# Kernel optimization log

Measured on AMD Instinct MI355X. Metric: run time of the kernel, lower is better.

## Reference

```python
import jax, jax.numpy as jnp
import numpy as np

N_QUBITS = 4
DIM = 16
N_QLAYERS = 2

def _cnot_perm(c, t):
    idx = np.arange(DIM)
    cbit = (idx >> (N_QUBITS - 1 - c)) & 1
    return np.where(cbit == 1, idx ^ (1 << (N_QUBITS - 1 - t)), idx)

# ring entanglement: CNOT(0,1), CNOT(1,2), CNOT(2,3), CNOT(3,0)
RING_PERMS = [jnp.asarray(_cnot_perm(i, (i + 1) % N_QUBITS)) for i in range(N_QUBITS)]
_idx = np.arange(DIM)
ZSIGNS = jnp.asarray(np.stack([1.0 - 2.0 * ((_idx >> (N_QUBITS - 1 - q)) & 1) for q in range(N_QUBITS)], axis=1).astype(np.float32))  # (16, 4)

def _rx(t):
    c = jnp.cos(t / 2).astype(jnp.complex64)
    s = jnp.sin(t / 2).astype(jnp.complex64)
    return jnp.stack([jnp.stack([c, -1j * s]), jnp.stack([-1j * s, c])])

def _ry(t):
    c = jnp.cos(t / 2).astype(jnp.complex64)
    s = jnp.sin(t / 2).astype(jnp.complex64)
    return jnp.stack([jnp.stack([c, -s]), jnp.stack([s, c])])

def _rz(t):
    e = jnp.exp(-0.5j * t.astype(jnp.complex64))
    z = jnp.zeros((), jnp.complex64)
    return jnp.stack([jnp.stack([e, z]), jnp.stack([z, jnp.conj(e)])])

def _apply_1q(state, g, q):
    # wire 0 is the most significant bit (PennyLane convention)
    s = state.reshape(2 ** q, 2, 2 ** (N_QUBITS - 1 - q))
    return jnp.einsum('ij,ajc->aic', g, s).reshape(DIM)

def _circuit(angles, qw):
    # angles: (4,), qw: (n_qlayers, 4, 3); returns PauliZ expvals (4,)
    state = jnp.zeros(DIM, jnp.complex64).at[0].set(1.0)
    for q in range(N_QUBITS):
        state = _apply_1q(state, _ry(angles[q]), q)
    for l in range(N_QLAYERS):
        for q in range(N_QUBITS):
            state = _apply_1q(state, _rx(qw[l, q, 0]), q)
            state = _apply_1q(state, _ry(qw[l, q, 1]), q)
            state = _apply_1q(state, _rz(qw[l, q, 2]), q)
        for p in RING_PERMS:
            state = state[p]
    probs = jnp.abs(state) ** 2
    return probs @ ZSIGNS

def _conv(x, w, b, stride, pad):
    y = jax.lax.conv_general_dilated(x, w, (stride, stride), [(pad, pad), (pad, pad)], dimension_numbers=('NCHW', 'OIHW', 'NCHW'))
    return y + b[None, :, None, None]

def _bn(x, g, b, m, v):
    scale = (g / jnp.sqrt(v + 1e-5))[None, :, None, None]
    return (x - m[None, :, None, None]) * scale + b[None, :, None, None]

def _forward(x, c1w, c1b, bn1g, bn1b, bn1m, bn1v, c2w, c2b, bn2g, bn2b, bn2m, bn2v, c3w, c3b, bn3g, bn3b, bn3m, bn3v, pre_w, pre_b, qw, pw1, pb1, pw2, pb2):
    B = x.shape[0]
    h = jax.nn.relu(_bn(_conv(x, c1w, c1b, 4, 3), bn1g, bn1b, bn1m, bn1v))   # (B,32,56,56)
    h = jax.nn.relu(_bn(_conv(h, c2w, c2b, 2, 1), bn2g, bn2b, bn2m, bn2v))   # (B,64,28,28)
    h = jax.nn.relu(_bn(_conv(h, c3w, c3b, 2, 1), bn3g, bn3b, bn3m, bn3v))   # (B,128,14,14)
    h = h.reshape(B, 128, 2, 7, 2, 7).mean(axis=(3, 5))                       # AdaptiveAvgPool2d((2,2))
    f = h.reshape(B, 128 * 4)
    ang = jnp.tanh(f @ pre_w.T + pre_b) * jnp.pi                              # (B,4)
    qout = jax.vmap(lambda a: _circuit(a, qw))(ang)                            # (B,4) batched statevector sim
    h1 = jax.nn.relu(qout @ pw1.T + pb1)                                       # dropout inactive (eval)
    return h1 @ pw2.T + pb2

def setup_inputs() -> dict:
    key = jax.random.key(0)
    ks = jax.random.split(key, 16)
    d = {
        'x': jax.random.normal(ks[0], (128, 3, 224, 224), jnp.float32),
        'c1w': jax.random.normal(ks[1], (32, 3, 7, 7), jnp.float32) * 0.05,
        'c1b': jax.random.normal(ks[2], (32,), jnp.float32) * 0.05,
        'bn1g': jnp.ones((32,), jnp.float32), 'bn1b': jnp.zeros((32,), jnp.float32),
        'bn1m': jnp.zeros((32,), jnp.float32), 'bn1v': jnp.ones((32,), jnp.float32),
        'c2w': jax.random.normal(ks[3], (64, 32, 3, 3), jnp.float32) * 0.05,
        'c2b': jax.random.normal(ks[4], (64,), jnp.float32) * 0.05,
        'bn2g': jnp.ones((64,), jnp.float32), 'bn2b': jnp.zeros((64,), jnp.float32),
        'bn2m': jnp.zeros((64,), jnp.float32), 'bn2v': jnp.ones((64,), jnp.float32),
        'c3w': jax.random.normal(ks[5], (128, 64, 3, 3), jnp.float32) * 0.05,
        'c3b': jax.random.normal(ks[6], (128,), jnp.float32) * 0.05,
        'bn3g': jnp.ones((128,), jnp.float32), 'bn3b': jnp.zeros((128,), jnp.float32),
        'bn3m': jnp.zeros((128,), jnp.float32), 'bn3v': jnp.ones((128,), jnp.float32),
        'pre_w': jax.random.normal(ks[7], (4, 512), jnp.float32) * 0.04,
        'pre_b': jax.random.normal(ks[8], (4,), jnp.float32) * 0.04,
        'qw': jax.random.normal(ks[9], (2, 4, 3), jnp.float32) * 0.1,
        'pw1': jax.random.normal(ks[10], (64, 4), jnp.float32) * 0.5,
        'pb1': jax.random.normal(ks[11], (64,), jnp.float32) * 0.5,
        'pw2': jax.random.normal(ks[12], (5, 64), jnp.float32) * 0.12,
        'pb2': jax.random.normal(ks[13], (5,), jnp.float32) * 0.12,
    }
    return d

def reference(x, c1w, c1b, bn1g, bn1b, bn1m, bn1v, c2w, c2b, bn2g, bn2b, bn2m, bn2v, c3w, c3b, bn3g, bn3b, bn3m, bn3v, pre_w, pre_b, qw, pw1, pb1, pw2, pb2):
    return _forward(x, c1w, c1b, bn1g, bn1b, bn1m, bn1v, c2w, c2b, bn2g, bn2b, bn2m, bn2v, c3w, c3b, bn3g, bn3b, bn3m, bn3v, pre_w, pre_b, qw, pw1, pb1, pw2, pb2)
```

## Files before the change

### kernel.cpp

```cpp
#include <hip/hip_runtime.h>
#include <math.h>

#define DEV __device__ __forceinline__

typedef __attribute__((ext_vector_type(8))) __bf16 bf16x8;
typedef __attribute__((ext_vector_type(4))) float f32x4;

__global__ void prep_weights(
    const float* __restrict__ c1w, const float* __restrict__ c1b,
    const float* __restrict__ g1, const float* __restrict__ b1,
    const float* __restrict__ m1, const float* __restrict__ v1,
    const float* __restrict__ c2w, const float* __restrict__ c2b,
    const float* __restrict__ g2, const float* __restrict__ b2,
    const float* __restrict__ m2, const float* __restrict__ v2,
    const float* __restrict__ c3w, const float* __restrict__ c3b,
    const float* __restrict__ g3, const float* __restrict__ b3,
    const float* __restrict__ m3, const float* __restrict__ v3,
    __bf16* __restrict__ wb1, __bf16* __restrict__ wb2, __bf16* __restrict__ wb3,
    float* __restrict__ sc1, float* __restrict__ sh1,
    float* __restrict__ sc2, float* __restrict__ sh2,
    float* __restrict__ sc3, float* __restrict__ sh3)
{
    int gid = blockIdx.x * 256 + threadIdx.x;
    int gs = gridDim.x * 256;
    for (int e = gid; e < 32 * 192; e += gs) {
        int oc = e / 192, k = e % 192, rr = k >> 3, kw = k & 7;
        wb1[e] = (rr < 21 && kw >= 1) ? (__bf16)c1w[oc * 147 + rr * 7 + kw - 1]
                                      : (__bf16)0.f;
    }
    for (int e = gid; e < 64 * 384; e += gs) {
        int oc = e / 384, k = e % 384, rr = k >> 2, kw = k & 3;
        wb2[e] = (kw >= 1) ? (__bf16)c2w[oc * 288 + rr * 3 + kw - 1] : (__bf16)0.f;
    }
    for (int e = gid; e < 128 * 768; e += gs) {
        int oc = e / 768, k = e % 768, rr = k >> 2, kw = k & 3;
        wb3[e] = (kw >= 1) ? (__bf16)c3w[oc * 576 + rr * 3 + kw - 1] : (__bf16)0.f;
    }
    if (gid < 32) {
        float s = g1[gid] * rsqrtf(v1[gid] + 1e-5f);
        sc1[gid] = s; sh1[gid] = (c1b[gid] - m1[gid]) * s + b1[gid];
    } else if (gid < 96) {
        int i = gid - 32;
        float s = g2[i] * rsqrtf(v2[i] + 1e-5f);
        sc2[i] = s; sh2[i] = (c2b[i] - m2[i]) * s + b2[i];
    } else if (gid < 224) {
        int i = gid - 96;
        float s = g3[i] * rsqrtf(v3[i] + 1e-5f);
        sc3[i] = s; sh3[i] = (c3b[i] - m3[i]) * s + b3[i];
    }
}

__global__ __launch_bounds__(256, 6) void conv1_kernel(
    const float* __restrict__ x,
    const __bf16* __restrict__ wb,
    const float* __restrict__ scale, const float* __restrict__ shift,
    __bf16* __restrict__ out)
{
    constexpr int IHW = 224 * 224, OHW = 56 * 56, LDR = 40;
    __shared__ __attribute__((aligned(16))) __bf16 Is[128 * LDR];
    __shared__ __attribute__((aligned(16))) __bf16 Ws[32 * LDR];

    const int tid = threadIdx.x;
    const int sb0 = blockIdx.x * 128;
    const int sm = tid & 127;
    const int kpb = tid >> 7;

    int a_n, a_ih0, a_iw0;
    {
        int m = sb0 + sm;
        a_n = m / OHW;
        int rem = m % OHW;
        a_ih0 = (rem / 56) * 4 - 3;
        a_iw0 = (rem % 56) * 4 - 3;
    }
    unsigned ihok = 0;
    #pragma unroll
    for (int t = 0; t < 7; ++t)
        ihok |= (unsigned)(((a_ih0 + t) >= 0) && ((a_ih0 + t) < 224)) << t;
    const bool left = (a_iw0 < 0);
    const int boff = a_n * 3 * IHW + a_ih0 * 224 + (a_iw0 - 1);

    const int w_oc = tid >> 2, w_j = tid & 3;
    const int wave = tid >> 6, lane = tid & 63;
    const int quad = lane >> 4, l16 = lane & 15;

    f32x4 acc[2][2] = {};

    #pragma unroll
    for (int ci = 0; ci < 6; ++ci) {
        const int k0 = ci * 32;
        bf16x8 hv[2];
        #pragma unroll
        for (int r = 0; r < 2; ++r) {
            const int rr = ci * 4 + kpb * 2 + r;
            if (rr >= 21) {
                hv[r] = (bf16x8){};
            } else {
                const int ic = rr / 7, kh = rr % 7;
                int off = boff + (ic * IHW + kh * 224);
                int o0 = off < 0 ? 0 : off;
                int o1 = (off + 4) < 0 ? 0 : (off + 4);
                float4 A = *(const float4*)(x + o0);
                float4 B = *(const float4*)(x + o1);
                float va[8] = {A.x, A.y, A.z, A.w, B.x, B.y, B.z, B.w};
                bool rok = (ihok >> kh) & 1u;
                #pragma unroll
                for (int j = 0; j < 8; ++j) va[j] = rok ? va[j] : 0.f;
                #pragma unroll
                for (int j = 1; j <= 3; ++j) va[j] = left ? 0.f : va[j];
                bf16x8 h;
                #pragma unroll
                for (int j = 0; j < 8; ++j) h[j] = (__bf16)va[j];
                hv[r] = h;
            }
        }
        bf16x8 wv = {};
        if (tid < 128)
            wv = *(const bf16x8*)&wb[(size_t)w_oc * 192 + k0 + w_j * 8];

        __syncthreads();
        *(bf16x8*)&Is[sm * LDR + kpb * 16]     = hv[0];
        *(bf16x8*)&Is[sm * LDR + kpb * 16 + 8] = hv[1];
        if (tid < 128) *(bf16x8*)&Ws[w_oc * LDR + w_j * 8] = wv;
        __syncthreads();

        bf16x8 afr[2], bfr[2];
        #pragma unroll
        for (int mt = 0; mt < 2; ++mt)
            afr[mt] = *(const bf16x8*)&Ws[(mt * 16 + l16) * LDR + quad * 8];
        #pragma unroll
        for (int nt = 0; nt < 2; ++nt)
            bfr[nt] = *(const bf16x8*)&Is[(wave * 32 + nt * 16 + l16) * LDR + quad * 8];
        #pragma unroll
        for (int mt = 0; mt < 2; ++mt)
            #pragma unroll
            for (int nt = 0; nt < 2; ++nt)
                acc[mt][nt] = __builtin_amdgcn_mfma_f32_16x16x32_bf16(
                    afr[mt], bfr[nt], acc[mt][nt], 0, 0, 0);
    }

    #pragma unroll
    for (int mt = 0; mt < 2; ++mt) {
        #pragma unroll
        for (int r = 0; r < 4; ++r) {
            int oc = mt * 16 + quad * 4 + r;
            float scl = scale[oc], shf = shift[oc];
            #pragma unroll
            for (int nt = 0; nt < 2; ++nt) {
                int sg = sb0 + wave * 32 + nt * 16 + l16;
                int n = sg / OHW, s = sg % OHW;
                float v = fmaf(acc[mt][nt][r], scl, shf);
                v = v > 0.f ? v : 0.f;
                out[((size_t)n * 32 + oc) * OHW + s] = (__bf16)v;
            }
        }
    }
}

template<typename OUTT, int NOCT, int IC, int KS, int RW, int S, int P,
         int IH, int IW, int OH, int OW, int OC, int KTP, int KCH, bool EPI>
DEV void conv_body(
    const __bf16* __restrict__ xo,
    const __bf16* __restrict__ wb,
    const float* __restrict__ scale, const float* __restrict__ shift,
    OUTT* __restrict__ out, __bf16* Is, __bf16* Ws)
{
    constexpr int KITER = KCH / 32;
    constexpr int OHW = OH * OW;
    constexpr int IHW = IH * IW;
    constexpr int LDR = 40;
    constexpr int NROW = 16 / RW;
    constexpr int RU = RW / 2;

    const int tid = threadIdx.x;
    const int sb0 = blockIdx.x * 128;
    const int oc0 = blockIdx.y * (NOCT * 16);

    const int sm = tid & 127;
    const int kpb = tid >> 7;
    int a_n, a_ih0, a_iw0;
    {
        int m = sb0 + sm;
        a_n = m / OHW;
        int rem = m % OHW;
        a_ih0 = (rem / OW) * S - P;
        a_iw0 = (rem % OW) * S - P;
    }
    unsigned ihok = 0;
    #pragma unroll
    for (int t = 0; t < KS; ++t)
        ihok |= (unsigned)(((a_ih0 + t) >= 0) && ((a_ih0 + t) < IH)) << t;
    const bool left = (a_iw0 < 0);
    const __bf16* xp = xo + ((size_t)a_n * IC * IHW + (ptrdiff_t)a_ih0 * IW
                             + (a_iw0 - 1));

    const int w_oc = tid >> 2, w_j = tid & 3;
    const int wave = tid >> 6, lane = tid & 63;
    const int quad = lane >> 4, l16 = lane & 15;

    f32x4 acc[NOCT][2] = {};

    #pragma unroll
    for (int ci = 0; ci < KITER; ++ci) {
        const int k0 = ci * 32;

        union { unsigned u[8]; bf16x8 v[2]; } Pk;
        #pragma unroll
        for (int r = 0; r < NROW; ++r) {
            const int rr = (k0 / RW) + kpb * NROW + r;
            if (rr >= IC * KS) {
                #pragma unroll
                for (int q = 0; q < RU; ++q) Pk.u[r * RU + q] = 0u;
            } else {
                const int ic = rr / KS, kh = rr % KS;
                const unsigned* rp = (const unsigned*)(xp + (ic * IHW + kh * IW));
                unsigned t[RU];
                #pragma unroll
                for (int q = 0; q < RU; ++q) t[q] = rp[q];
                bool rok = (ihok >> kh) & 1u;
                #pragma unroll
                for (int q = 0; q < RU; ++q) t[q] = rok ? t[q] : 0u;
                t[0] = left ? (t[0] & 0x0000FFFFu) : t[0];
                if constexpr (P >= 2) t[1] = left ? 0u : t[1];
                #pragma unroll
                for (int q = 0; q < RU; ++q) Pk.u[r * RU + q] = t[q];
            }
        }
        bf16x8 wv = {};
        if (NOCT == 4 || tid < 128)
            wv = *(const bf16x8*)&wb[(size_t)(oc0 + w_oc) * KTP + k0 + w_j * 8];

        __syncthreads();
        *(bf16x8*)&Is[sm * LDR + kpb * 16]     = Pk.v[0];
        *(bf16x8*)&Is[sm * LDR + kpb * 16 + 8] = Pk.v[1];
        if (NOCT == 4 || tid < 128) *(bf16x8*)&Ws[w_oc * LDR + w_j * 8] = wv;
        __syncthreads();

        bf16x8 afr[NOCT], bfr[2];
        #pragma unroll
        for (int mt = 0; mt < NOCT; ++mt)
            afr[mt] = *(const bf16x8*)&Ws[(mt * 16 + l16) * LDR + quad * 8];
        #pragma unroll
        for (int nt = 0; nt < 2; ++nt)
            bfr[nt] = *(const bf16x8*)&Is[(wave * 32 + nt * 16 + l16) * LDR + quad * 8];
        #pragma unroll
        for (int mt = 0; mt < NOCT; ++mt)
            #pragma unroll
            for (int nt = 0; nt < 2; ++nt)
                acc[mt][nt] = __builtin_amdgcn_mfma_f32_16x16x32_bf16(
                    afr[mt], bfr[nt], acc[mt][nt], 0, 0, 0);
    }

    #pragma unroll
    for (int mt = 0; mt < NOCT; ++mt) {
        #pragma unroll
        for (int r = 0; r < 4; ++r) {
            int oc = oc0 + mt * 16 + quad * 4 + r;
            float scl = EPI ? scale[oc] : 0.f;
            float shf = EPI ? shift[oc] : 0.f;
            #pragma unroll
            for (int nt = 0; nt < 2; ++nt) {
                int sg = sb0 + wave * 32 + nt * 16 + l16;
                int n = sg / OHW, s = sg % OHW;
                float v = acc[mt][nt][r];
                if (EPI) {
                    v = fmaf(v, scl, shf);
                    v = v > 0.f ? v : 0.f;
                }
                out[((size_t)n * OC + oc) * OHW + s] = (OUTT)v;
            }
        }
    }
}

__global__ __launch_bounds__(256, 4) void conv2_kernel(
    const __bf16* __restrict__ xo, const __bf16* __restrict__ wb,
    const float* __restrict__ scale, const float* __restrict__ shift,
    __bf16* __restrict__ out)
{
    __shared__ __attribute__((aligned(16))) __bf16 Is[128 * 40];
    __shared__ __attribute__((aligned(16))) __bf16 Ws[64 * 40];
    conv_body<__bf16, 4, 32, 3, 4, 2, 1, 56, 56, 28, 28, 64, 384, 384, true>(
        xo, wb, scale, shift, out, Is, Ws);
}

__global__ __launch_bounds__(256, 6) void conv3_kernel(
    const __bf16* __restrict__ xo, const __bf16* __restrict__ wb,
    const float* __restrict__ scale, const float* __restrict__ shift,
    __bf16* __restrict__ out)
{
    __shared__ __attribute__((aligned(16))) __bf16 Is[128 * 40];
    __shared__ __attribute__((aligned(16))) __bf16 Ws[32 * 40];
    conv_body<__bf16, 2, 64, 3, 4, 2, 1, 28, 28, 14, 14, 128, 768, 768, true>(
        xo, wb, scale, shift, out, Is, Ws);
}

__global__ __launch_bounds__(256) void pool_kernel(
    const __bf16* __restrict__ c3o,
    float* __restrict__ f)
{
    int idx = blockIdx.x * 256 + threadIdx.x;
    int b = idx >> 9, p = idx & 511;
    int c = p >> 2, i = (p >> 1) & 1, j = p & 1;
    size_t base = ((size_t)b * 128 + c) * 196 + (i * 7) * 14 + j * 7;
    float s = 0.f;
    #pragma unroll
    for (int u = 0; u < 7; ++u)
        #pragma unroll
        for (int v = 0; v < 7; ++v)
            s += (float)c3o[base + u * 14 + v];
    f[idx] = s * (1.f / 49.f);
}

__global__ __launch_bounds__(256) void head_kernel(
    const float* __restrict__ fpool,
    const float* __restrict__ pre_w, const float* __restrict__ pre_b,
    const float* __restrict__ qw,
    const float* __restrict__ pw1, const float* __restrict__ pb1,
    const float* __restrict__ pw2, const float* __restrict__ pb2,
    float* __restrict__ out)
{
    __shared__ float f[512];
    __shared__ float ang[4];
    __shared__ float zexp[4];
    __shared__ float h1[64];

    int b = blockIdx.x;
    int t = threadIdx.x;

    for (int p = t; p < 512; p += 256) f[p] = fpool[b * 512 + p];
    __syncthreads();

    int wv = t >> 6, lane = t & 63;
    float partial = 0.f;
    for (int d = lane; d < 512; d += 64)
        partial += f[d] * pre_w[wv * 512 + d];
    #pragma unroll
    for (int off = 32; off > 0; off >>= 1)
        partial += __shfl_down(partial, off, 64);
    if (lane == 0)
        ang[wv] = tanhf(partial + pre_b[wv]) * 3.14159265358979323846f;
    __syncthreads();

    if (t == 0) {
        float re[16], im[16];
        #pragma unroll
        for (int i = 0; i < 16; ++i) { re[i] = 0.f; im[i] = 0.f; }
        re[0] = 1.f;

        #pragma unroll
        for (int q = 0; q < 4; ++q) {
            const int mask = 8 >> q;
            float c = cosf(ang[q] * 0.5f), s = sinf(ang[q] * 0.5f);
            #pragma unroll
            for (int i = 0; i < 16; ++i) {
                if (i & mask) continue;
                const int j = i | mask;
                float r0 = re[i], i0 = im[i], r1 = re[j], i1 = im[j];
                re[i] = c * r0 - s * r1;  im[i] = c * i0 - s * i1;
                re[j] = s * r0 + c * r1;  im[j] = s * i0 + c * i1;
            }
        }
        #pragma unroll
        for (int l = 0; l < 2; ++l) {
            #pragma unroll
            for (int q = 0; q < 4; ++q) {
                const int mask = 8 >> q;
                const float* qq = qw + (l * 4 + q) * 3;
                {
                    float c = cosf(qq[0] * 0.5f), s = sinf(qq[0] * 0.5f);
                    #pragma unroll
                    for (int i = 0; i < 16; ++i) {
                        if (i & mask) continue;
                        const int j = i | mask;
                        float r0 = re[i], i0 = im[i], r1 = re[j], i1 = im[j];
                        re[i] = c * r0 + s * i1;  im[i] = c * i0 - s * r1;
                        re[j] = s * i0 + c * r1;  im[j] = -s * r0 + c * i1;
                    }
                }
                {
                    float c = cosf(qq[1] * 0.5f), s = sinf(qq[1] * 0.5f);
                    #pragma unroll
                    for (int i = 0; i < 16; ++i) {
                        if (i & mask) continue;
                        const int j = i | mask;
                        float r0 = re[i], i0 = im[i], r1 = re[j], i1 = im[j];
                        re[i] = c * r0 - s * r1;  im[i] = c * i0 - s * i1;
                        re[j] = s * r0 + c * r1;  im[j] = s * i0 + c * i1;
                    }
                }
                {
                    float c = cosf(qq[2] * 0.5f), s = sinf(qq[2] * 0.5f);
                    #pragma unroll
                    for (int i = 0; i < 16; ++i) {
                        float sg = (i & mask) ? s : -s;
                        float r = re[i], m = im[i];
                        re[i] = c * r - sg * m;
                        im[i] = c * m + sg * r;
                    }
                }
            }
            #pragma unroll
            for (int e = 0; e < 4; ++e) {
                const int cm = 8 >> e, tm = 8 >> ((e + 1) & 3);
                #pragma unroll
                for (int i = 0; i < 16; ++i) {
                    if ((i & cm) && !(i & tm)) {
                        const int j = i | tm;
                        float r = re[i]; re[i] = re[j]; re[j] = r;
                        float m = im[i]; im[i] = im[j]; im[j] = m;
                    }
                }
            }
        }
        #pragma unroll
        for (int q = 0; q < 4; ++q) {
            const int mask = 8 >> q;
            float z = 0.f;
            #pragma unroll
            for (int i = 0; i < 16; ++i) {
                float p2 = re[i] * re[i] + im[i] * im[i];
                z += (i & mask) ? -p2 : p2;
            }
            zexp[q] = z;
        }
    }
    __syncthreads();

    if (t < 64) {
        float s = pb1[t];
        #pragma unroll
        for (int k = 0; k < 4; ++k) s += zexp[k] * pw1[t * 4 + k];
        h1[t] = s > 0.f ? s : 0.f;
    }
    __syncthreads();

    if (t < 5) {
        float s = pb2[t];
        for (int k = 0; k < 64; ++k) s += h1[k] * pw2[t * 64 + k];
        out[b * 5 + t] = s;
    }
}

extern "C" void kernel_launch(void* const* d_in, const int* in_sizes, int n_in,
                              void* d_out, int out_size, void* d_ws, size_t ws_size,
                              hipStream_t stream) {
    const float* x    = (const float*)d_in[0];
    const float* c1w  = (const float*)d_in[1];
    const float* c1b  = (const float*)d_in[2];
    const float* bn1g = (const float*)d_in[3];
    const float* bn1b = (const float*)d_in[4];
    const float* bn1m = (const float*)d_in[5];
    const float* bn1v = (const float*)d_in[6];
    const float* c2w  = (const float*)d_in[7];
    const float* c2b  = (const float*)d_in[8];
    const float* bn2g = (const float*)d_in[9];
    const float* bn2b = (const float*)d_in[10];
    const float* bn2m = (const float*)d_in[11];
    const float* bn2v = (const float*)d_in[12];
    const float* c3w  = (const float*)d_in[13];
    const float* c3bi = (const float*)d_in[14];
    const float* bn3g = (const float*)d_in[15];
    const float* bn3b = (const float*)d_in[16];
    const float* bn3m = (const float*)d_in[17];
    const float* bn3v = (const float*)d_in[18];
    const float* prw  = (const float*)d_in[19];
    const float* prb  = (const float*)d_in[20];
    const float* qw   = (const float*)d_in[21];
    const float* pw1  = (const float*)d_in[22];
    const float* pb1  = (const float*)d_in[23];
    const float* pw2  = (const float*)d_in[24];
    const float* pb2  = (const float*)d_in[25];

    const int N = in_sizes[0] / (3 * 224 * 224);
    const size_t NC1 = (size_t)N * 32 * 56 * 56;
    const size_t NC2 = (size_t)N * 64 * 28 * 28;
    const size_t NC3 = (size_t)N * 128 * 14 * 14;

    __bf16* ws_h = (__bf16*)d_ws;
    __bf16* c1o = ws_h + 64;
    __bf16* c2o = ws_h + 64 + NC1 + 64 + 64;
    __bf16* c3o = ws_h + 64 + NC1 + 64 + 64 + NC2 + 64;
    __bf16* wb1 = c3o + NC3;
    __bf16* wb2 = wb1 + 32 * 192;
    __bf16* wb3 = wb2 + 64 * 384;
    float* sc1 = (float*)(wb3 + 128 * 768);
    float* sh1 = sc1 + 32;
    float* sc2 = sh1 + 32;  float* sh2 = sc2 + 64;
    float* sc3 = sh2 + 64;  float* sh3 = sc3 + 128;
    float* fpool = sh3 + 128;

    prep_weights<<<192, 256, 0, stream>>>(
        c1w, c1b, bn1g, bn1b, bn1m, bn1v,
        c2w, c2b, bn2g, bn2b, bn2m, bn2v,
        c3w, c3bi, bn3g, bn3b, bn3m, bn3v,
        wb1, wb2, wb3, sc1, sh1, sc2, sh2, sc3, sh3);

    conv1_kernel<<<dim3(401408 / 128, 1), 256, 0, stream>>>(x, wb1, sc1, sh1, c1o);
    conv2_kernel<<<dim3(100352 / 128, 1), 256, 0, stream>>>(c1o, wb2, sc2, sh2, c2o);
    conv3_kernel<<<dim3(25088 / 128, 4), 256, 0, stream>>>(c2o, wb3, sc3, sh3, c3o);

    pool_kernel<<<(N * 512) / 256, 256, 0, stream>>>(c3o, fpool);
    head_kernel<<<N, 256, 0, stream>>>(fpool, prw, prb, qw,
                                       pw1, pb1, pw2, pb2, (float*)d_out);
}
```

Measured before the change: 246.3 us.

## Double K-chunk per barrier in conv kernels and fold pooling into head

The conv1, conv2 and conv3 kernels now stage a 64-wide K slice per iteration instead of 32. This halves the number of syncthreads round trips and issues two MFMA k-steps per shared-memory fill, with the LDS row pitch widened to 72 to match. The separate adaptive-pool kernel is removed and its averaging is done inside the head kernel, which drops one launch and the intermediate buffer. In exchange, more registers and LDS are used per block, which may lower occupancy, and the pooling loads now run inside only N head blocks.

```diff
diff --git a/kernel.cpp b/kernel.cpp
--- a/kernel.cpp
+++ b/kernel.cpp
@@ -56,7 +56,7 @@
     const float* __restrict__ scale, const float* __restrict__ shift,
     __bf16* __restrict__ out)
 {
-    constexpr int IHW = 224 * 224, OHW = 56 * 56, LDR = 40;
+    constexpr int IHW = 224 * 224, OHW = 56 * 56, LDR = 72;
     __shared__ __attribute__((aligned(16))) __bf16 Is[128 * LDR];
     __shared__ __attribute__((aligned(16))) __bf16 Ws[32 * LDR];
 
@@ -80,19 +80,19 @@
     const bool left = (a_iw0 < 0);
     const int boff = a_n * 3 * IHW + a_ih0 * 224 + (a_iw0 - 1);
 
-    const int w_oc = tid >> 2, w_j = tid & 3;
+    const int w_oc = tid >> 3, w_j = tid & 7;
     const int wave = tid >> 6, lane = tid & 63;
     const int quad = lane >> 4, l16 = lane & 15;
 
     f32x4 acc[2][2] = {};
 
     #pragma unroll
-    for (int ci = 0; ci < 6; ++ci) {
-        const int k0 = ci * 32;
-        bf16x8 hv[2];
-        #pragma unroll
-        for (int r = 0; r < 2; ++r) {
-            const int rr = ci * 4 + kpb * 2 + r;
+    for (int ci = 0; ci < 3; ++ci) {
+        const int k0 = ci * 64;
+        bf16x8 hv[4];
+        #pragma unroll
+        for (int r = 0; r < 4; ++r) {
+            const int rr = ci * 8 + kpb * 4 + r;
             if (rr >= 21) {
                 hv[r] = (bf16x8){};
             } else {
@@ -114,29 +114,31 @@
                 hv[r] = h;
             }
         }
-        bf16x8 wv = {};
-        if (tid < 128)
-            wv = *(const bf16x8*)&wb[(size_t)w_oc * 192 + k0 + w_j * 8];
+        bf16x8 wv = *(const bf16x8*)&wb[(size_t)w_oc * 192 + k0 + w_j * 8];
 
         __syncthreads();
-        *(bf16x8*)&Is[sm * LDR + kpb * 16]     = hv[0];
-        *(bf16x8*)&Is[sm * LDR + kpb * 16 + 8] = hv[1];
-        if (tid < 128) *(bf16x8*)&Ws[w_oc * LDR + w_j * 8] = wv;
+        #pragma unroll
+        for (int r = 0; r < 4; ++r)
+            *(bf16x8*)&Is[sm * LDR + kpb * 32 + r * 8] = hv[r];
+        *(bf16x8*)&Ws[w_oc * LDR + w_j * 8] = wv;
         __syncthreads();
 
-        bf16x8 afr[2], bfr[2];
-        #pragma unroll
-        for (int mt = 0; mt < 2; ++mt)
-            afr[mt] = *(const bf16x8*)&Ws[(mt * 16 + l16) * LDR + quad * 8];
-        #pragma unroll
-        for (int nt = 0; nt < 2; ++nt)
-            bfr[nt] = *(const bf16x8*)&Is[(wave * 32 + nt * 16 + l16) * LDR + quad * 8];
-        #pragma unroll
-        for (int mt = 0; mt < 2; ++mt)
+        #pragma unroll
+        for (int kk = 0; kk < 2; ++kk) {
+            bf16x8 afr[2], bfr[2];
+            #pragma unroll
+            for (int mt = 0; mt < 2; ++mt)
+                afr[mt] = *(const bf16x8*)&Ws[(mt * 16 + l16) * LDR + kk * 32 + quad * 8];
             #pragma unroll
             for (int nt = 0; nt < 2; ++nt)
-                acc[mt][nt] = __builtin_amdgcn_mfma_f32_16x16x32_bf16(
-                    afr[mt], bfr[nt], acc[mt][nt], 0, 0, 0);
+                bfr[nt] = *(const bf16x8*)&Is[(wave * 32 + nt * 16 + l16) * LDR + kk * 32 + quad * 8];
+            #pragma unroll
+            for (int mt = 0; mt < 2; ++mt)
+                #pragma unroll
+                for (int nt = 0; nt < 2; ++nt)
+                    acc[mt][nt] = __builtin_amdgcn_mfma_f32_16x16x32_bf16(
+                        afr[mt], bfr[nt], acc[mt][nt], 0, 0, 0);
+        }
     }
 
     #pragma unroll
@@ -157,20 +159,20 @@
     }
 }
 
-template<typename OUTT, int NOCT, int IC, int KS, int RW, int S, int P,
-         int IH, int IW, int OH, int OW, int OC, int KTP, int KCH, bool EPI>
-DEV void conv_body(
+template<int NOCT, int IC, int IH, int IW, int OH, int OW, int OC,
+         int KTP, int KCH>
+DEV void conv_body64(
     const __bf16* __restrict__ xo,
     const __bf16* __restrict__ wb,
     const float* __restrict__ scale, const float* __restrict__ shift,
-    OUTT* __restrict__ out, __bf16* Is, __bf16* Ws)
-{
-    constexpr int KITER = KCH / 32;
+    __bf16* __restrict__ out, __bf16* Is, __bf16* Ws)
+{
+    constexpr int KS = 3, S = 2, P = 1;
+    constexpr int KITER = KCH / 64;
     constexpr int OHW = OH * OW;
     constexpr int IHW = IH * IW;
-    constexpr int LDR = 40;
-    constexpr int NROW = 16 / RW;
-    constexpr int RU = RW / 2;
+    constexpr int LDR = 72;
+    constexpr int WLD = NOCT / 2;
 
     const int tid = threadIdx.x;
     const int sb0 = blockIdx.x * 128;
@@ -194,7 +196,6 @@
     const __bf16* xp = xo + ((size_t)a_n * IC * IHW + (ptrdiff_t)a_ih0 * IW
                              + (a_iw0 - 1));
 
-    const int w_oc = tid >> 2, w_j = tid & 3;
     const int wave = tid >> 6, lane = tid & 63;
     const int quad = lane >> 4, l16 = lane & 15;
 
@@ -202,53 +203,56 @@
 
     #pragma unroll
     for (int ci = 0; ci < KITER; ++ci) {
-        const int k0 = ci * 32;
-
-        union { unsigned u[8]; bf16x8 v[2]; } Pk;
-        #pragma unroll
-        for (int r = 0; r < NROW; ++r) {
-            const int rr = (k0 / RW) + kpb * NROW + r;
-            if (rr >= IC * KS) {
-                #pragma unroll
-                for (int q = 0; q < RU; ++q) Pk.u[r * RU + q] = 0u;
-            } else {
-                const int ic = rr / KS, kh = rr % KS;
-                const unsigned* rp = (const unsigned*)(xp + (ic * IHW + kh * IW));
-                unsigned t[RU];
-                #pragma unroll
-                for (int q = 0; q < RU; ++q) t[q] = rp[q];
-                bool rok = (ihok >> kh) & 1u;
-                #pragma unroll
-                for (int q = 0; q < RU; ++q) t[q] = rok ? t[q] : 0u;
-                t[0] = left ? (t[0] & 0x0000FFFFu) : t[0];
-                if constexpr (P >= 2) t[1] = left ? 0u : t[1];
-                #pragma unroll
-                for (int q = 0; q < RU; ++q) Pk.u[r * RU + q] = t[q];
-            }
-        }
-        bf16x8 wv = {};
-        if (NOCT == 4 || tid < 128)
-            wv = *(const bf16x8*)&wb[(size_t)(oc0 + w_oc) * KTP + k0 + w_j * 8];
+        const int k0 = ci * 64;
+
+        union { unsigned u[16]; bf16x8 v[4]; } Pk;
+        #pragma unroll
+        for (int r = 0; r < 8; ++r) {
+            const int rr = (k0 / 4) + kpb * 8 + r;
+            const int ic = rr / KS, kh = rr % KS;
+            const unsigned* rp = (const unsigned*)(xp + (ic * IHW + kh * IW));
+            unsigned t0 = rp[0], t1 = rp[1];
+            bool rok = (ihok >> kh) & 1u;
+            t0 = rok ? t0 : 0u;
+            t1 = rok ? t1 : 0u;
+            t0 = left ? (t0 & 0x0000FFFFu) : t0;
+            Pk.u[r * 2]     = t0;
+            Pk.u[r * 2 + 1] = t1;
+        }
+        bf16x8 wv[WLD];
+        #pragma unroll
+        for (int i = 0; i < WLD; ++i) {
+            int e = i * 256 + tid;
+            wv[i] = *(const bf16x8*)&wb[(size_t)(oc0 + (e >> 3)) * KTP + k0 + (e & 7) * 8];
+        }
 
         __syncthreads();
-        *(bf16x8*)&Is[sm * LDR + kpb * 16]     = Pk.v[0];
-        *(bf16x8*)&Is[sm * LDR + kpb * 16 + 8] = Pk.v[1];
-        if (NOCT == 4 || tid < 128) *(bf16x8*)&Ws[w_oc * LDR + w_j * 8] = wv;
+        #pragma unroll
+        for (int q = 0; q < 4; ++q)
+            *(bf16x8*)&Is[sm * LDR + kpb * 32 + q * 8] = Pk.v[q];
+        #pragma unroll
+        for (int i = 0; i < WLD; ++i) {
+            int e = i * 256 + tid;
+            *(bf16x8*)&Ws[(e >> 3) * LDR + (e & 7) * 8] = wv[i];
+        }
         __syncthreads();
 
-        bf16x8 afr[NOCT], bfr[2];
-        #pragma unroll
-        for (int mt = 0; mt < NOCT; ++mt)
-            afr[mt] = *(const bf16x8*)&Ws[(mt * 16 + l16) * LDR + quad * 8];
-        #pragma unroll
-        for (int nt = 0; nt < 2; ++nt)
-            bfr[nt] = *(const bf16x8*)&Is[(wave * 32 + nt * 16 + l16) * LDR + quad * 8];
-        #pragma unroll
-        for (int mt = 0; mt < NOCT; ++mt)
+        #pragma unroll
+        for (int kk = 0; kk < 2; ++kk) {
+            bf16x8 afr[NOCT], bfr[2];
+            #pragma unroll
+            for (int mt = 0; mt < NOCT; ++mt)
+                afr[mt] = *(const bf16x8*)&Ws[(mt * 16 + l16) * LDR + kk * 32 + quad * 8];
             #pragma unroll
             for (int nt = 0; nt < 2; ++nt)
-                acc[mt][nt] = __builtin_amdgcn_mfma_f32_16x16x32_bf16(
-                    afr[mt], bfr[nt], acc[mt][nt], 0, 0, 0);
+                bfr[nt] = *(const bf16x8*)&Is[(wave * 32 + nt * 16 + l16) * LDR + kk * 32 + quad * 8];
+            #pragma unroll
+            for (int mt = 0; mt < NOCT; ++mt)
+                #pragma unroll
+                for (int nt = 0; nt < 2; ++nt)
+                    acc[mt][nt] = __builtin_amdgcn_mfma_f32_16x16x32_bf16(
+                        afr[mt], bfr[nt], acc[mt][nt], 0, 0, 0);
+        }
     }
 
     #pragma unroll
@@ -256,18 +260,14 @@
         #pragma unroll
         for (int r = 0; r < 4; ++r) {
             int oc = oc0 + mt * 16 + quad * 4 + r;
-            float scl = EPI ? scale[oc] : 0.f;
-            float shf = EPI ? shift[oc] : 0.f;
+            float scl = scale[oc], shf = shift[oc];
             #pragma unroll
             for (int nt = 0; nt < 2; ++nt) {
                 int sg = sb0 + wave * 32 + nt * 16 + l16;
                 int n = sg / OHW, s = sg % OHW;
-                float v = acc[mt][nt][r];
-                if (EPI) {
-                    v = fmaf(v, scl, shf);
-                    v = v > 0.f ? v : 0.f;
-                }
-                out[((size_t)n * OC + oc) * OHW + s] = (OUTT)v;
+                float v = fmaf(acc[mt][nt][r], scl, shf);
+                v = v > 0.f ? v : 0.f;
+                out[((size_t)n * OC + oc) * OHW + s] = (__bf16)v;
             }
         }
     }
@@ -278,9 +278,9 @@
     const float* __restrict__ scale, const float* __restrict__ shift,
     __bf16* __restrict__ out)
 {
-    __shared__ __attribute__((aligned(16))) __bf16 Is[128 * 40];
-    __shared__ __attribute__((aligned(16))) __bf16 Ws[64 * 40];
-    conv_body<__bf16, 4, 32, 3, 4, 2, 1, 56, 56, 28, 28, 64, 384, 384, true>(
+    __shared__ __attribute__((aligned(16))) __bf16 Is[128 * 72];
+    __shared__ __attribute__((aligned(16))) __bf16 Ws[64 * 72];
+    conv_body64<4, 32, 56, 56, 28, 28, 64, 384, 384>(
         xo, wb, scale, shift, out, Is, Ws);
 }
 
@@ -289,31 +289,14 @@
     const float* __restrict__ scale, const float* __restrict__ shift,
     __bf16* __restrict__ out)
 {
-    __shared__ __attribute__((aligned(16))) __bf16 Is[128 * 40];
-    __shared__ __attribute__((aligned(16))) __bf16 Ws[32 * 40];
-    conv_body<__bf16, 2, 64, 3, 4, 2, 1, 28, 28, 14, 14, 128, 768, 768, true>(
+    __shared__ __attribute__((aligned(16))) __bf16 Is[128 * 72];
+    __shared__ __attribute__((aligned(16))) __bf16 Ws[32 * 72];
+    conv_body64<2, 64, 28, 28, 14, 14, 128, 768, 768>(
         xo, wb, scale, shift, out, Is, Ws);
 }
 
-__global__ __launch_bounds__(256) void pool_kernel(
+__global__ __launch_bounds__(256) void head_kernel(
     const __bf16* __restrict__ c3o,
-    float* __restrict__ f)
-{
-    int idx = blockIdx.x * 256 + threadIdx.x;
-    int b = idx >> 9, p = idx & 511;
-    int c = p >> 2, i = (p >> 1) & 1, j = p & 1;
-    size_t base = ((size_t)b * 128 + c) * 196 + (i * 7) * 14 + j * 7;
-    float s = 0.f;
-    #pragma unroll
-    for (int u = 0; u < 7; ++u)
-        #pragma unroll
-        for (int v = 0; v < 7; ++v)
-            s += (float)c3o[base + u * 14 + v];
-    f[idx] = s * (1.f / 49.f);
-}
-
-__global__ __launch_bounds__(256) void head_kernel(
-    const float* __restrict__ fpool,
     const float* __restrict__ pre_w, const float* __restrict__ pre_b,
     const float* __restrict__ qw,
     const float* __restrict__ pw1, const float* __restrict__ pb1,
@@ -328,7 +311,17 @@
     int b = blockIdx.x;
     int t = threadIdx.x;
 
-    for (int p = t; p < 512; p += 256) f[p] = fpool[b * 512 + p];
+    for (int p = t; p < 512; p += 256) {
+        int c = p >> 2, i = (p >> 1) & 1, j = p & 1;
+        size_t base = ((size_t)b * 128 + c) * 196 + (i * 7) * 14 + j * 7;
+        float s = 0.f;
+        #pragma unroll
+        for (int u = 0; u < 7; ++u)
+            #pragma unroll
+            for (int v = 0; v < 7; ++v)
+                s += (float)c3o[base + u * 14 + v];
+        f[p] = s * (1.f / 49.f);
+    }
     __syncthreads();
 
     int wv = t >> 6, lane = t & 63;
@@ -488,7 +481,6 @@
     float* sh1 = sc1 + 32;
     float* sc2 = sh1 + 32;  float* sh2 = sc2 + 64;
     float* sc3 = sh2 + 64;  float* sh3 = sc3 + 128;
-    float* fpool = sh3 + 128;
 
     prep_weights<<<192, 256, 0, stream>>>(
         c1w, c1b, bn1g, bn1b, bn1m, bn1v,
@@ -500,7 +492,6 @@
     conv2_kernel<<<dim3(100352 / 128, 1), 256, 0, stream>>>(c1o, wb2, sc2, sh2, c2o);
     conv3_kernel<<<dim3(25088 / 128, 4), 256, 0, stream>>>(c2o, wb3, sc3, sh3, c3o);
 
-    pool_kernel<<<(N * 512) / 256, 256, 0, stream>>>(c3o, fpool);
-    head_kernel<<<N, 256, 0, stream>>>(fpool, prw, prb, qw,
+    head_kernel<<<N, 256, 0, stream>>>(c3o, prw, prb, qw,
                                        pw1, pb1, pw2, pb2, (float*)d_out);
 }
```

After: 240.3 us. 2.4% less time.
